# Kernel optimization log

Hardware: AMD Instinct MI355X
Metric: run time of the kernel (lower is better)

The kernel has to match this reference:

```python
import jax, jax.numpy as jnp
import numpy as np
from jax import lax

# dims
B, T, N, E, DEG = 8, 24, 1000, 1000, 20
F_IN, C_RAW, DM, HC, TK, PRED, OUT = 16, 8, 32, 32, 32, 12, 1
LAM = 0.3
EPS = 1e-8


def _dyn_features(x_raw):
    # build_window_dynamic_features: per-node window stats (mean, std) -> (B, N, 2C)
    return jnp.concatenate([x_raw.mean(axis=1), x_raw.std(axis=1)], axis=-1)


def _dynamic_weights(x_raw, W, members, centers, offsets):
    feat = _dyn_features(x_raw)                      # (B, N, D)
    M = members.shape[0]
    # member -> owning edge id from CSR offsets (jit-safe repeat_interleave)
    mids = jnp.searchsorted(offsets[1:], jnp.arange(M), side='right')  # (M,)
    mf = feat[:, members, :]                          # (B, M, D)
    cf = feat[:, centers[mids], :]                    # (B, M, D)
    sim = (mf * cf).sum(-1) / (jnp.linalg.norm(mf, axis=-1) * jnp.linalg.norm(cf, axis=-1) + EPS)
    sim = jnp.clip(sim, 0.0, 1.0)                     # (B, M)
    counts = (offsets[1:] - offsets[:-1]).astype(sim.dtype)  # (E,)
    mean_sim = jnp.zeros((sim.shape[0], offsets.shape[0] - 1), sim.dtype).at[:, mids].add(sim)
    mean_sim = mean_sim / jnp.clip(counts, 1.0)[None, :]
    smin = mean_sim.min(axis=1, keepdims=True)
    smax = mean_sim.max(axis=1, keepdims=True)
    mean_sim = (mean_sim - smin) / (smax - smin + EPS)
    return W[None, :] * (1.0 + LAM * mean_sim)        # (B, E)


def _norm_hypergraph(H, Wd):
    # A = Dv^{-1/2} H W De^{-1} H^T Dv^{-1/2}, batched over edge weights Wd (B,E)
    De = jnp.clip(H.sum(axis=0), 1.0)                 # (E,)
    dv = jnp.einsum('ne,be->bn', H, Wd)               # (B, N)
    dvi = lax.rsqrt(jnp.clip(dv, EPS))
    HW = H[None, :, :] * (Wd / De)[:, None, :]        # (B, N, E)
    A0 = jnp.einsum('bne,me->bnm', HW, H)             # (B, N, N)
    return dvi[:, :, None] * A0 * dvi[:, None, :]


def _lstm_last(seq, wx, wh, b):
    # TKANLayer temporal recurrence (LSTM-style cell), return_sequences=False
    BN = seq.shape[0]
    Hd = wh.shape[0]
    h0 = jnp.zeros((BN, Hd), seq.dtype)

    def step(carry, xt):
        h, c = carry
        z = xt @ wx + h @ wh + b                      # (BN, 4H)
        i, f, g, o = jnp.split(z, 4, axis=-1)
        c = jax.nn.sigmoid(f) * c + jax.nn.sigmoid(i) * jnp.tanh(g)
        h = jax.nn.sigmoid(o) * jnp.tanh(c)
        return (h, c), None

    (h, _), _ = lax.scan(step, (h0, h0), jnp.swapaxes(seq, 0, 1))
    return h


def setup_inputs() -> dict:
    key = jax.random.key(0)
    ks = jax.random.split(key, 16)

    edge_members = jax.random.randint(ks[0], (E * DEG,), 0, N)
    edge_centers = jnp.arange(E)                      # center node = edge index
    edge_offsets = jnp.arange(E + 1) * DEG            # uniform-degree CSR
    mids = jnp.repeat(jnp.arange(E), DEG)
    H = (jnp.zeros((N, E))
         .at[edge_members, mids].set(1.0)
         .at[edge_centers, jnp.arange(E)].set(1.0))
    W = jax.random.uniform(ks[1], (E,), minval=0.5, maxval=1.5)

    x = jax.random.normal(ks[2], (B, T, N, F_IN))
    x_raw = jax.random.normal(ks[3], (B, T, N, C_RAW))

    w = lambda k, s: jax.random.normal(k, s) * 0.05
    return {
        'x': x, 'x_raw': x_raw, 'H': H, 'W': W,
        'edge_members': edge_members, 'edge_centers': edge_centers, 'edge_offsets': edge_offsets,
        'in_proj_w': w(ks[4], (F_IN, DM)), 'in_proj_b': jnp.zeros((DM,)),
        'conv_w': w(ks[5], (DM, HC)), 'conv_b': jnp.zeros((HC,)),
        'lstm_wx': w(ks[6], (HC, 4 * TK)), 'lstm_wh': w(ks[7], (TK, 4 * TK)), 'lstm_b': jnp.zeros((4 * TK,)),
        'head_w1': w(ks[8], (TK, TK)), 'head_b1': jnp.zeros((TK,)),
        'head_w2': w(ks[9], (TK, PRED * OUT)), 'head_b2': jnp.zeros((PRED * OUT,)),
        'output_length': 12,
    }


def reference(x, x_raw, H, W, edge_members, edge_centers, edge_offsets,
              in_proj_w, in_proj_b, conv_w, conv_b,
              lstm_wx, lstm_wh, lstm_b,
              head_w1, head_b1, head_w2, head_b2, output_length):
    xp = x @ in_proj_w + in_proj_b                    # (B, T, N, DM)

    # DynamicEdgeWeighter is @torch.no_grad() in the original
    Wd = lax.stop_gradient(_dynamic_weights(x_raw, W, edge_members, edge_centers, edge_offsets))
    A = _norm_hypergraph(H, Wd)                       # (B, N, N)

    # per-timestep hypergraph conv, vectorized over T (same math as the Python loop)
    h = jnp.einsum('bnm,btmf->btnf', A, xp)
    h = jax.nn.silu(h @ conv_w + conv_b)              # (B, T, N, HC)

    seq = jnp.transpose(h, (0, 2, 1, 3)).reshape(B * N, T, HC)
    ht = _lstm_last(seq, lstm_wx, lstm_wh, lstm_b)    # (B*N, TK)

    y = jax.nn.silu(ht @ head_w1 + head_b1) @ head_w2 + head_b2
    y = y.reshape(B, N, PRED, OUT).transpose(0, 2, 1, 3)  # (B, PRED, N, OUT)
    return y[:, :output_length]
```

## Files before the change

### kernel.cpp

```cpp
#include <hip/hip_runtime.h>
#include <hip/hip_bf16.h>
#include <math.h>

#define BB 8
#define TT 24
#define NN 1000
#define EE 1000
#define DEG 20
#define FIN 16
#define CRAW 8
#define DM 32
#define HCN 32
#define TKN 32
#define PREDN 12
#define LAMF 0.3f
#define EPSF 1e-8f

typedef float f4 __attribute__((ext_vector_type(4)));

__device__ __forceinline__ float sigmoidf_(float x){ return 1.f/(1.f+__expf(-x)); }
__device__ __forceinline__ float siluf_(float x){ return x/(1.f+__expf(-x)); }
__device__ __forceinline__ float sigmfast_(float x){
  return __builtin_amdgcn_rcpf(1.f+__expf(-x));
}
__device__ __forceinline__ float tanhfast_(float x){
  float xx = fminf(fmaxf(x,-15.f),15.f);
  float e = __expf(2.f*xx);
  return 1.f - 2.f*__builtin_amdgcn_rcpf(e+1.f);
}

__global__ void k_dedup(const int* __restrict__ members, const int* __restrict__ centers,
                        const int* __restrict__ offsets,
                        int* __restrict__ edge_nodes, int* __restrict__ edge_cnt,
                        int* __restrict__ node_deg){
  int e = blockIdx.x*blockDim.x + threadIdx.x;
  if(e>=EE) return;
  int st=offsets[e], en=offsets[e+1];
  int c=centers[e];
  int mem[DEG];
  #pragma unroll
  for(int k=0;k<DEG;k++) mem[k] = (st+k<en)? members[st+k] : -1;
  edge_nodes[e*(DEG+1)+0]=c;
  atomicAdd(&node_deg[c],1);
  int cnt=1;
  #pragma unroll
  for(int k=0;k<DEG;k++){
    int m = mem[k];
    bool dup = (m==c) | (m<0);
    #pragma unroll
    for(int k2=0;k2<DEG;k2++) if(k2<k && mem[k2]==m) dup=true;
    if(!dup){
      edge_nodes[e*(DEG+1)+cnt]=m;
      atomicAdd(&node_deg[m],1);
      cnt++;
    }
  }
  edge_cnt[e]=cnt;
  for(int j=cnt;j<DEG+1;j++) edge_nodes[e*(DEG+1)+j]=0;
}

__global__ __launch_bounds__(1024) void k_scan(const int* __restrict__ node_deg,
                                               int* __restrict__ node_off){
  __shared__ int buf[1024];
  int i=threadIdx.x;
  buf[i] = (i<NN)? node_deg[i]:0;
  __syncthreads();
  for(int d=1;d<1024;d<<=1){
    int v = (i>=d)? buf[i-d] : 0;
    __syncthreads();
    buf[i]+=v;
    __syncthreads();
  }
  if(i==0) node_off[0]=0;
  if(i<NN) node_off[i+1]=buf[i];
}

__global__ void k_fill(const int* __restrict__ edge_nodes, const int* __restrict__ edge_cnt,
                       const int* __restrict__ node_off, int* __restrict__ cursor,
                       int* __restrict__ node_edges){
  int e = blockIdx.x*blockDim.x + threadIdx.x;
  if(e>=EE) return;
  int cnt=edge_cnt[e];
  for(int j=0;j<cnt;j++){
    int n = edge_nodes[e*(DEG+1)+j];
    int pos = atomicAdd(&cursor[n],1);
    node_edges[node_off[n]+pos] = e;
  }
}

__global__ void k_feat(const float* __restrict__ xraw, float* __restrict__ feat){
  int tid = threadIdx.x;
  int c = tid & 7, nloc = tid >> 3;
  int row = blockIdx.x*32 + nloc;
  if (row >= BB*NN) return;
  int b = row/NN, n = row%NN;
  float s=0.f, s2=0.f;
  for (int t=0;t<TT;t++){
    float vv = xraw[(((size_t)(b*TT+t)*NN + n)*CRAW) + c];
    s += vv; s2 += vv*vv;
  }
  float m = s*(1.f/TT);
  float var = fmaxf(s2*(1.f/TT) - m*m, 0.f);
  feat[(size_t)row*16 + c]     = m;
  feat[(size_t)row*16 + 8 + c] = sqrtf(var);
}

__global__ __launch_bounds__(256) void k_sim1(
    const float* __restrict__ feat,
    const int* __restrict__ members, const int* __restrict__ centers,
    const int* __restrict__ offsets, float* __restrict__ ms)
{
  int tid = threadIdx.x;
  int lane2 = tid & 3;
  int task = blockIdx.x*64 + (tid>>2);
  if(task >= BB*EE) return;
  int b = task/EE, e = task%EE;
  const float* fb = feat + (size_t)b*NN*16;
  int st=offsets[e], en=offsets[e+1];
  int ci=centers[e];
  float cf[16]; float nc=0.f;
  const f4* cp = (const f4*)(fb + ci*16);
  #pragma unroll
  for(int k=0;k<4;k++){
    f4 v = cp[k];
    #pragma unroll
    for(int c=0;c<4;c++){ cf[4*k+c]=v[c]; nc = fmaf(v[c],v[c],nc); }
  }
  nc = sqrtf(nc);
  float acc=0.f;
  for(int k=st+lane2;k<en;k+=4){
    int m=members[k];
    const f4* mp = (const f4*)(fb + m*16);
    float dot=0.f, nm=0.f;
    #pragma unroll
    for(int kk=0;kk<4;kk++){
      f4 v = mp[kk];
      #pragma unroll
      for(int c=0;c<4;c++){ dot = fmaf(v[c], cf[4*kk+c], dot); nm = fmaf(v[c],v[c],nm); }
    }
    float sim = dot/(sqrtf(nm)*nc + EPSF);
    acc += fminf(fmaxf(sim,0.f),1.f);
  }
  acc += __shfl_xor(acc, 1, 64);
  acc += __shfl_xor(acc, 2, 64);
  if(lane2==0) ms[task] = acc / fmaxf((float)(en-st),1.f);
}

__global__ __launch_bounds__(1024) void k_sim2dv(
    const float* __restrict__ ms, const float* __restrict__ W,
    const int* __restrict__ node_off, const int* __restrict__ node_edges,
    float* __restrict__ Wd, float* __restrict__ dvi)
{
  __shared__ float red1[1024], red2[1024];
  __shared__ float wdl[EE];
  int b = blockIdx.x;
  int tid = threadIdx.x;
  float msv = (tid<EE)? ms[b*EE+tid] : 0.f;
  red1[tid]=(tid<EE)? msv : 1e30f;
  red2[tid]=(tid<EE)? msv : -1e30f;
  __syncthreads();
  for(int s=512;s>0;s>>=1){
    if(tid<s){
      red1[tid]=fminf(red1[tid],red1[tid+s]);
      red2[tid]=fmaxf(red2[tid],red2[tid+s]);
    }
    __syncthreads();
  }
  if(tid<EE){
    float msn=(msv-red1[0])/(red2[0]-red1[0]+EPSF);
    float w = W[tid]*(1.f+LAMF*msn);
    Wd[b*EE+tid]=w;
    wdl[tid]=w;
  }
  __syncthreads();
  if(tid<NN){
    int st=node_off[tid], en=node_off[tid+1];
    float dv=0.f;
    for(int k=st;k<en;k++) dv += wdl[node_edges[k]];
    dvi[b*NN+tid] = rsqrtf(fmaxf(dv, EPSF));
  }
}

__global__ __launch_bounds__(1024) void k_slice(
    const float* __restrict__ x,
    const float* __restrict__ ipw, const float* __restrict__ ipb,
    const float* __restrict__ dvi, const float* __restrict__ Wd,
    const int* __restrict__ edge_nodes, const int* __restrict__ edge_cnt,
    const int* __restrict__ node_off, const int* __restrict__ node_edges,
    const float* __restrict__ cw, const float* __restrict__ cb,
    float* __restrict__ hc_out)
{
  __shared__ f4 zbuf[NN*8];
  __shared__ float ipws[FIN*32];
  __shared__ f4 cws4[DM*8];
  __shared__ float wde[EE];
  __shared__ int   cnts[EE];
  __shared__ float ipbs[32], cbs[32];

  int tid = threadIdx.x;
  int bt  = blockIdx.x;
  int b = bt / TT, t = bt % TT;

  for(int i=tid;i<FIN*32;i+=1024) ipws[i]=ipw[i];
  for(int i=tid;i<DM*8;i+=1024) cws4[i]=((const f4*)cw)[i];
  for(int e=tid;e<EE;e+=1024){
    int c = edge_cnt[e];
    cnts[e]=c;
    wde[e]=Wd[b*EE+e]/(float)c;
  }
  if(tid<32){ ipbs[tid]=ipb[tid]; cbs[tid]=cb[tid]; }
  __syncthreads();

  const float* xb  = x + (size_t)bt*NN*FIN;
  const float* dvb = dvi + b*NN;
  float* zs = (float*)zbuf;

  {
    int g = tid>>5, f = tid&31;
    for(int p=0;p<32;p++){
      int r = p*32+g;
      if(r<NN){
        const f4* x4 = (const f4*)(xb + r*FIN);
        float acc = ipbs[f];
        #pragma unroll
        for(int k=0;k<4;k++){
          f4 xv = x4[k];
          acc = fmaf(xv[0], ipws[(4*k+0)*32+f], acc);
          acc = fmaf(xv[1], ipws[(4*k+1)*32+f], acc);
          acc = fmaf(xv[2], ipws[(4*k+2)*32+f], acc);
          acc = fmaf(xv[3], ipws[(4*k+3)*32+f], acc);
        }
        zs[r*32 + (((f>>2)^(r&7))<<2) + (f&3)] = dvb[r]*acc;
      }
    }
  }
  __syncthreads();

  int grp = tid>>3, q = tid&7;
  f4 vreg[8];
  #pragma unroll
  for(int p=0;p<8;p++){
    int e = p*128 + grp;
    f4 acc = (f4)0.f;
    if(e<EE){
      int cnt = cnts[e];
      const int* enp = edge_nodes + e*(DEG+1);
      int idx[DEG+1];
      #pragma unroll
      for(int j=0;j<DEG+1;j++) idx[j]=enp[j];
      #pragma unroll
      for(int j=0;j<DEG+1;j++){
        f4 v = zbuf[idx[j]*8 + (q ^ (idx[j]&7))];
        if(j<cnt) acc += v;
      }
      acc *= wde[e];
    }
    vreg[p]=acc;
  }
  __syncthreads();
  #pragma unroll
  for(int p=0;p<8;p++){
    int e = p*128 + grp;
    if(e<EE) zbuf[e*8 + (q^(e&7))] = vreg[p];
  }
  __syncthreads();

  int lanew = tid&63, grpw = lanew>>3;
  for(int p=0;p<8;p++){
    int n = p*128 + grp;
    int st=0, deg=0;
    if(n<NN){ st=node_off[n]; deg=node_off[n+1]-st; }
    int idx[24];
    #pragma unroll
    for(int k=0;k<24;k++) idx[k] = (k<deg)? node_edges[st+k] : 0;
    f4 acc = (f4)0.f;
    #pragma unroll
    for(int k=0;k<24;k++){
      int e2 = idx[k];
      f4 v = zbuf[e2*8 + (q ^ (e2&7))];
      if(k<deg) acc += v;
    }
    for(int j=st+24;j<st+deg;j++){
      int e2 = node_edges[j];
      acc += zbuf[e2*8 + (q ^ (e2&7))];
    }
    float dvn = (n<NN)? dvb[n] : 0.f;
    acc *= dvn;
    f4 hcq;
    #pragma unroll
    for(int c=0;c<4;c++) hcq[c]=cbs[q*4+c];
    #pragma unroll
    for(int i=0;i<32;i++){
      float h2i = __shfl(acc[i&3], grpw*8 + (i>>2), 64);
      f4 w = cws4[i*8+q];
      hcq += h2i * w;
    }
    #pragma unroll
    for(int c=0;c<4;c++) hcq[c]=siluf_(hcq[c]);
    if(n<NN) ((f4*)hc_out)[ ((size_t)(b*NN+n)*TT + t)*8 + q ] = hcq;
  }
}

__global__ __launch_bounds__(256) void k_zx(
    const float* __restrict__ hc, const float* __restrict__ wx,
    const float* __restrict__ lb, float* __restrict__ zx)
{
  __shared__ f4 wxl[32*32];
  __shared__ f4 hcl[64*8];
  __shared__ f4 lbl[32];
  int tid = threadIdx.x;
  for(int w=tid;w<1024;w+=256) wxl[w] = ((const f4*)wx)[w];
  if(tid<32) lbl[tid] = ((const f4*)lb)[tid];
  size_t base = (size_t)blockIdx.x*64;
  {
    const f4* hp = (const f4*)(hc + base*32);
    hcl[tid]     = hp[tid];
    hcl[tid+256] = hp[tid+256];
  }
  __syncthreads();
  int ig = tid>>5, q4 = tid&31;
  f4 acc[8];
  f4 l = lbl[q4];
  #pragma unroll
  for(int it=0;it<8;it++) acc[it]=l;
  #pragma unroll
  for(int c=0;c<8;c++){
    f4 w0 = wxl[(4*c+0)*32+q4];
    f4 w1 = wxl[(4*c+1)*32+q4];
    f4 w2 = wxl[(4*c+2)*32+q4];
    f4 w3 = wxl[(4*c+3)*32+q4];
    #pragma unroll
    for(int it=0;it<8;it++){
      f4 h4 = hcl[(ig*8+it)*8 + c];
      acc[it] += h4[0]*w0;
      acc[it] += h4[1]*w1;
      acc[it] += h4[2]*w2;
      acc[it] += h4[3]*w3;
    }
  }
  #pragma unroll
  for(int it=0;it<8;it++){
    ((f4*)(zx + (base + (size_t)(ig*8+it))*128))[q4] = acc[it];
  }
}

__global__ __launch_bounds__(256,2) void k_lstm(const float* __restrict__ zx,
    const float* __restrict__ wh,
    const float* __restrict__ w1, const float* __restrict__ b1,
    const float* __restrict__ w2, const float* __restrict__ b2,
    float* __restrict__ out){
  __shared__ float hsh[8*32];
  int tid = threadIdx.x;
  int r = tid>>5, c = tid&31;
  int row = blockIdx.x*8 + r;
  const float* zr = zx + (size_t)row*TT*128;
  float wr0[32], wr1[32], wr2[32], wr3[32];
  #pragma unroll
  for(int i=0;i<32;i++){
    wr0[i]=wh[i*128 + c];
    wr1[i]=wh[i*128 + 32 + c];
    wr2[i]=wh[i*128 + 64 + c];
    wr3[i]=wh[i*128 + 96 + c];
  }
  const f4* hrow4 = (const f4*)&hsh[r*32];
  float h=0.f, cs=0.f;
  float p0=zr[c], p1=zr[32+c], p2=zr[64+c], p3=zr[96+c];
  for(int t=0;t<TT;t++){
    float z0=p0, z1=p1, z2=p2, z3=p3;
    if(t+1<TT){
      const float* nz = zr + (size_t)(t+1)*128;
      p0=nz[c]; p1=nz[32+c]; p2=nz[64+c]; p3=nz[96+c];
    }
    hsh[r*32+c] = h;
    #pragma unroll
    for(int i4=0;i4<8;i4++){
      f4 h4 = hrow4[i4];
      #pragma unroll
      for(int k=0;k<4;k++){
        int i = i4*4+k;
        z0 = fmaf(h4[k], wr0[i], z0);
        z1 = fmaf(h4[k], wr1[i], z1);
        z2 = fmaf(h4[k], wr2[i], z2);
        z3 = fmaf(h4[k], wr3[i], z3);
      }
    }
    float ig = sigmfast_(z0);
    float fg = sigmfast_(z1);
    float gg = tanhfast_(z2);
    float og = sigmfast_(z3);
    cs = fg*cs + ig*gg;
    h = og*tanhfast_(cs);
  }
  int b = row/NN, n = row%NN;
  hsh[r*32+c] = h;
  float t1 = b1[c];
  #pragma unroll
  for(int i4=0;i4<8;i4++){
    f4 h4 = hrow4[i4];
    #pragma unroll
    for(int k=0;k<4;k++) t1 = fmaf(h4[k], w1[(i4*4+k)*32+c], t1);
  }
  t1 = siluf_(t1);
  hsh[r*32+c] = t1;
  float y = (c<PREDN)? b2[c] : 0.f;
  #pragma unroll
  for(int i4=0;i4<8;i4++){
    f4 t4 = hrow4[i4];
    #pragma unroll
    for(int k=0;k<4;k++){
      if(c<PREDN) y = fmaf(t4[k], w2[(i4*4+k)*PREDN+c], y);
    }
  }
  if(c<PREDN) out[((size_t)b*PREDN + c)*NN + n] = y;
}

extern "C" void kernel_launch(void* const* d_in, const int* in_sizes, int n_in,
                              void* d_out, int out_size, void* d_ws, size_t ws_size,
                              hipStream_t stream) {
  const float* x       = (const float*)d_in[0];
  const float* xraw    = (const float*)d_in[1];
  const float* W       = (const float*)d_in[3];
  const int*   members = (const int*)d_in[4];
  const int*   centers = (const int*)d_in[5];
  const int*   offsets = (const int*)d_in[6];
  const float* ipw     = (const float*)d_in[7];
  const float* ipb     = (const float*)d_in[8];
  const float* cw      = (const float*)d_in[9];
  const float* cb      = (const float*)d_in[10];
  const float* wx      = (const float*)d_in[11];
  const float* wh      = (const float*)d_in[12];
  const float* lb      = (const float*)d_in[13];
  const float* w1      = (const float*)d_in[14];
  const float* b1      = (const float*)d_in[15];
  const float* w2      = (const float*)d_in[16];
  const float* b2      = (const float*)d_in[17];
  float* out = (float*)d_out;

  float* zx   = (float*)d_ws;
  float* hc   = zx + 24576000;
  float* feat = hc + 6144000;
  float* ms   = feat + 128000;
  float* Wd   = ms + 8000;
  float* dvi  = Wd + 8000;
  int* edge_nodes = (int*)(dvi + 8000);
  int* edge_cnt   = edge_nodes + 21000;
  int* node_off   = edge_cnt + 1000;
  int* node_deg   = node_off + 1001;
  int* cursor     = node_deg + 1000;
  int* node_edges = cursor + 1000;

  hipMemsetAsync(node_deg, 0, 2000*sizeof(int), stream);

  k_feat<<<250, 256, 0, stream>>>(xraw, feat);
  k_dedup<<<(EE+255)/256, 256, 0, stream>>>(members, centers, offsets,
                                            edge_nodes, edge_cnt, node_deg);
  k_scan<<<1, 1024, 0, stream>>>(node_deg, node_off);
  k_fill<<<(EE+255)/256, 256, 0, stream>>>(edge_nodes, edge_cnt, node_off,
                                           cursor, node_edges);
  k_sim1<<<125, 256, 0, stream>>>(feat, members, centers, offsets, ms);
  k_sim2dv<<<BB, 1024, 0, stream>>>(ms, W, node_off, node_edges, Wd, dvi);
  k_slice<<<BB*TT, 1024, 0, stream>>>(x, ipw, ipb, dvi, Wd,
                                      edge_nodes, edge_cnt, node_off, node_edges,
                                      cw, cb, hc);
  k_zx<<<3000, 256, 0, stream>>>(hc, wx, lb, zx);
  k_lstm<<<(BB*NN)/8, 256, 0, stream>>>(zx, wh, w1, b1, w2, b2, out);
}
```

Before: 279.8 us.

## Split hypergraph slice across feature halves and fuse conv into zx kernel

k_slice now launches two blocks per (b,t), each handling 16 of the 32 projected features. This halves LDS use per block and allows two blocks per CU, while also doubling the block count. The conv_w matmul and SiLU move out of k_slice into k_zx, which now reads the raw aggregated features and applies the conv before the LSTM input projection. The dedup and fill launches switch to smaller blocks. In exchange, each half-block recomputes the gathers and reloads the edge metadata, and k_zx does extra work per tile.

```diff
diff --git a/kernel.cpp b/kernel.cpp
--- a/kernel.cpp
+++ b/kernel.cpp
@@ -181,34 +181,33 @@
   }
 }
 
-__global__ __launch_bounds__(1024) void k_slice(
+__global__ __launch_bounds__(1024,2) void k_slice(
     const float* __restrict__ x,
     const float* __restrict__ ipw, const float* __restrict__ ipb,
     const float* __restrict__ dvi, const float* __restrict__ Wd,
     const int* __restrict__ edge_nodes, const int* __restrict__ edge_cnt,
     const int* __restrict__ node_off, const int* __restrict__ node_edges,
-    const float* __restrict__ cw, const float* __restrict__ cb,
-    float* __restrict__ hc_out)
+    float* __restrict__ h2g)
 {
-  __shared__ f4 zbuf[NN*8];
-  __shared__ float ipws[FIN*32];
-  __shared__ f4 cws4[DM*8];
+  __shared__ f4 zbuf[NN*4];
   __shared__ float wde[EE];
   __shared__ int   cnts[EE];
-  __shared__ float ipbs[32], cbs[32];
-
-  int tid = threadIdx.x;
-  int bt  = blockIdx.x;
+  __shared__ float ipws[FIN*16];
+  __shared__ float ipbs[16];
+
+  int tid = threadIdx.x;
+  int blk = blockIdx.x;
+  int bt = blk >> 1, half = blk & 1;
   int b = bt / TT, t = bt % TT;
-
-  for(int i=tid;i<FIN*32;i+=1024) ipws[i]=ipw[i];
-  for(int i=tid;i<DM*8;i+=1024) cws4[i]=((const f4*)cw)[i];
+  int coff = half << 4;
+
+  for(int i=tid;i<FIN*16;i+=1024){ int row=i>>4, c=i&15; ipws[i]=ipw[row*32 + coff + c]; }
+  if(tid<16) ipbs[tid]=ipb[coff+tid];
   for(int e=tid;e<EE;e+=1024){
     int c = edge_cnt[e];
     cnts[e]=c;
     wde[e]=Wd[b*EE+e]/(float)c;
   }
-  if(tid<32){ ipbs[tid]=ipb[tid]; cbs[tid]=cb[tid]; }
   __syncthreads();
 
   const float* xb  = x + (size_t)bt*NN*FIN;
@@ -216,42 +215,46 @@
   float* zs = (float*)zbuf;
 
   {
-    int g = tid>>5, f = tid&31;
-    for(int p=0;p<32;p++){
-      int r = p*32+g;
+    int g = tid>>4, f = tid&15;
+    int q = f>>2, l = f&3;
+    for(int p=0;p<16;p++){
+      int r = p*64+g;
       if(r<NN){
-        const f4* x4 = (const f4*)(xb + r*FIN);
+        const f4* x4 = (const f4*)(xb + (size_t)r*FIN);
         float acc = ipbs[f];
         #pragma unroll
         for(int k=0;k<4;k++){
           f4 xv = x4[k];
-          acc = fmaf(xv[0], ipws[(4*k+0)*32+f], acc);
-          acc = fmaf(xv[1], ipws[(4*k+1)*32+f], acc);
-          acc = fmaf(xv[2], ipws[(4*k+2)*32+f], acc);
-          acc = fmaf(xv[3], ipws[(4*k+3)*32+f], acc);
+          acc = fmaf(xv[0], ipws[(4*k+0)*16+f], acc);
+          acc = fmaf(xv[1], ipws[(4*k+1)*16+f], acc);
+          acc = fmaf(xv[2], ipws[(4*k+2)*16+f], acc);
+          acc = fmaf(xv[3], ipws[(4*k+3)*16+f], acc);
         }
-        zs[r*32 + (((f>>2)^(r&7))<<2) + (f&3)] = dvb[r]*acc;
+        zs[r*16 + ((q ^ ((r>>1)&3))<<2) + l] = dvb[r]*acc;
       }
     }
   }
   __syncthreads();
 
-  int grp = tid>>3, q = tid&7;
-  f4 vreg[8];
-  #pragma unroll
-  for(int p=0;p<8;p++){
-    int e = p*128 + grp;
+  int grp = tid>>2, q = tid&3;
+  f4 vreg[4];
+  #pragma unroll
+  for(int p=0;p<4;p++){
+    int e = p*256 + grp;
     f4 acc = (f4)0.f;
     if(e<EE){
       int cnt = cnts[e];
       const int* enp = edge_nodes + e*(DEG+1);
-      int idx[DEG+1];
-      #pragma unroll
-      for(int j=0;j<DEG+1;j++) idx[j]=enp[j];
-      #pragma unroll
-      for(int j=0;j<DEG+1;j++){
-        f4 v = zbuf[idx[j]*8 + (q ^ (idx[j]&7))];
-        if(j<cnt) acc += v;
+      for(int j0=0;j0<DEG+1;j0+=8){
+        int idx[8];
+        #pragma unroll
+        for(int k=0;k<8;k++) idx[k] = (j0+k<DEG+1)? enp[j0+k] : 0;
+        #pragma unroll
+        for(int k=0;k<8;k++){
+          int m = idx[k];
+          f4 v = zbuf[m*4 + (q ^ ((m>>1)&3))];
+          if(j0+k<cnt) acc += v;
+        }
       }
       acc *= wde[e];
     }
@@ -259,63 +262,75 @@
   }
   __syncthreads();
   #pragma unroll
-  for(int p=0;p<8;p++){
-    int e = p*128 + grp;
-    if(e<EE) zbuf[e*8 + (q^(e&7))] = vreg[p];
-  }
-  __syncthreads();
-
-  int lanew = tid&63, grpw = lanew>>3;
-  for(int p=0;p<8;p++){
-    int n = p*128 + grp;
-    int st=0, deg=0;
-    if(n<NN){ st=node_off[n]; deg=node_off[n+1]-st; }
-    int idx[24];
-    #pragma unroll
-    for(int k=0;k<24;k++) idx[k] = (k<deg)? node_edges[st+k] : 0;
-    f4 acc = (f4)0.f;
-    #pragma unroll
-    for(int k=0;k<24;k++){
-      int e2 = idx[k];
-      f4 v = zbuf[e2*8 + (q ^ (e2&7))];
-      if(k<deg) acc += v;
-    }
-    for(int j=st+24;j<st+deg;j++){
-      int e2 = node_edges[j];
-      acc += zbuf[e2*8 + (q ^ (e2&7))];
-    }
-    float dvn = (n<NN)? dvb[n] : 0.f;
-    acc *= dvn;
-    f4 hcq;
-    #pragma unroll
-    for(int c=0;c<4;c++) hcq[c]=cbs[q*4+c];
-    #pragma unroll
-    for(int i=0;i<32;i++){
-      float h2i = __shfl(acc[i&3], grpw*8 + (i>>2), 64);
-      f4 w = cws4[i*8+q];
-      hcq += h2i * w;
-    }
-    #pragma unroll
-    for(int c=0;c<4;c++) hcq[c]=siluf_(hcq[c]);
-    if(n<NN) ((f4*)hc_out)[ ((size_t)(b*NN+n)*TT + t)*8 + q ] = hcq;
+  for(int p=0;p<4;p++){
+    int e = p*256 + grp;
+    if(e<EE) zbuf[e*4 + (q^((e>>1)&3))] = vreg[p];
+  }
+  __syncthreads();
+
+  #pragma unroll
+  for(int p=0;p<4;p++){
+    int n = p*256 + grp;
+    if(n<NN){
+      int st=node_off[n], deg=node_off[n+1]-st;
+      f4 acc = (f4)0.f;
+      for(int j0=0;j0<deg;j0+=8){
+        int idx[8];
+        int m8 = deg - j0;
+        #pragma unroll
+        for(int k=0;k<8;k++) idx[k] = (k<m8)? node_edges[st+j0+k] : 0;
+        #pragma unroll
+        for(int k=0;k<8;k++){
+          int e2 = idx[k];
+          f4 v = zbuf[e2*4 + (q ^ ((e2>>1)&3))];
+          if(k<m8) acc += v;
+        }
+      }
+      acc *= dvb[n];
+      ((f4*)(h2g + (((size_t)(b*NN+n))*TT + t)*32 + coff))[q] = acc;
+    }
   }
 }
 
 __global__ __launch_bounds__(256) void k_zx(
-    const float* __restrict__ hc, const float* __restrict__ wx,
-    const float* __restrict__ lb, float* __restrict__ zx)
+    const float* __restrict__ h2, const float* __restrict__ cw,
+    const float* __restrict__ cb,
+    const float* __restrict__ wx, const float* __restrict__ lb,
+    float* __restrict__ zx)
 {
   __shared__ f4 wxl[32*32];
+  __shared__ f4 cwl[32*8];
+  __shared__ float hl[64*36];
   __shared__ f4 hcl[64*8];
   __shared__ f4 lbl[32];
+  __shared__ f4 cbl[8];
   int tid = threadIdx.x;
   for(int w=tid;w<1024;w+=256) wxl[w] = ((const f4*)wx)[w];
+  if(tid<256) cwl[tid] = ((const f4*)cw)[tid];
   if(tid<32) lbl[tid] = ((const f4*)lb)[tid];
+  if(tid<8)  cbl[tid] = ((const f4*)cb)[tid];
   size_t base = (size_t)blockIdx.x*64;
   {
-    const f4* hp = (const f4*)(hc + base*32);
-    hcl[tid]     = hp[tid];
-    hcl[tid+256] = hp[tid+256];
+    const f4* hp = (const f4*)(h2 + base*32);
+    #pragma unroll
+    for(int rep=0;rep<2;rep++){
+      int w = tid + rep*256;
+      int it = w>>3, qc = w&7;
+      *(f4*)&hl[it*36 + qc*4] = hp[w];
+    }
+  }
+  __syncthreads();
+  #pragma unroll
+  for(int rep=0;rep<2;rep++){
+    int task = tid + rep*256;
+    int it = task>>3, qc = task&7;
+    const float* hrow = &hl[it*36];
+    f4 a = cbl[qc];
+    #pragma unroll
+    for(int i=0;i<32;i++) a += hrow[i]*cwl[i*8+qc];
+    #pragma unroll
+    for(int c=0;c<4;c++) a[c]=siluf_(a[c]);
+    hcl[it*8+qc]=a;
   }
   __syncthreads();
   int ig = tid>>5, q4 = tid&31;
@@ -437,8 +452,8 @@
   float* out = (float*)d_out;
 
   float* zx   = (float*)d_ws;
-  float* hc   = zx + 24576000;
-  float* feat = hc + 6144000;
+  float* h2g  = zx + 24576000;
+  float* feat = h2g + 6144000;
   float* ms   = feat + 128000;
   float* Wd   = ms + 8000;
   float* dvi  = Wd + 8000;
@@ -452,16 +467,16 @@
   hipMemsetAsync(node_deg, 0, 2000*sizeof(int), stream);
 
   k_feat<<<250, 256, 0, stream>>>(xraw, feat);
-  k_dedup<<<(EE+255)/256, 256, 0, stream>>>(members, centers, offsets,
-                                            edge_nodes, edge_cnt, node_deg);
+  k_dedup<<<16, 64, 0, stream>>>(members, centers, offsets,
+                                 edge_nodes, edge_cnt, node_deg);
   k_scan<<<1, 1024, 0, stream>>>(node_deg, node_off);
-  k_fill<<<(EE+255)/256, 256, 0, stream>>>(edge_nodes, edge_cnt, node_off,
-                                           cursor, node_edges);
+  k_fill<<<16, 64, 0, stream>>>(edge_nodes, edge_cnt, node_off,
+                                cursor, node_edges);
   k_sim1<<<125, 256, 0, stream>>>(feat, members, centers, offsets, ms);
   k_sim2dv<<<BB, 1024, 0, stream>>>(ms, W, node_off, node_edges, Wd, dvi);
-  k_slice<<<BB*TT, 1024, 0, stream>>>(x, ipw, ipb, dvi, Wd,
-                                      edge_nodes, edge_cnt, node_off, node_edges,
-                                      cw, cb, hc);
-  k_zx<<<3000, 256, 0, stream>>>(hc, wx, lb, zx);
+  k_slice<<<BB*TT*2, 1024, 0, stream>>>(x, ipw, ipb, dvi, Wd,
+                                        edge_nodes, edge_cnt, node_off, node_edges,
+                                        h2g);
+  k_zx<<<3000, 256, 0, stream>>>(h2g, cw, cb, wx, lb, zx);
   k_lstm<<<(BB*NN)/8, 256, 0, stream>>>(zx, wh, w1, b1, w2, b2, out);
 }
```

Result: faster. 273.2 us (-2.4%).
